# Optimization experiments

Hardware: AMD Instinct MI355X
Metric: run time of the kernel (lower is better)

Reference implementation:

```python
import jax, jax.numpy as jnp
import numpy as np

MARGIN = 0.2
BIG = 1e9  # sentinel for masked (positive-pair) entries in the row-min


def setup_inputs() -> dict:
    key = jax.random.key(0)
    k1, k2, k3 = jax.random.split(key, 3)
    B, D, NUM_CLASSES = 4096, 512, 1000
    z_s = jax.random.normal(k1, (B, D), dtype=jnp.float32)
    z_i = jax.random.normal(k2, (B, D), dtype=jnp.float32)
    labels = jax.random.randint(k3, (B,), 0, NUM_CLASSES, dtype=jnp.int64)
    return {"z_s": z_s, "z_i": z_i, "labels": labels}


def reference(z_s, z_i, labels):
    # dists[a, b] = 1 - <z_s[a], z_i[b]>   -- [B, B]
    dists = 1.0 - jnp.einsum("ad,bd->ab", z_s, z_i)
    pos_mask = labels[:, None] == labels[None, :]  # [B, B] same-label pairs

    p = jnp.diagonal(dists)  # positive distance per anchor, [B]
    # hardest negative per anchor: min over entries with different label
    n = jnp.min(jnp.where(pos_mask, BIG, dists), axis=1)  # [B]
    has_neg = ~jnp.all(pos_mask, axis=1)  # anchors with at least one negative

    per_anchor = jax.nn.relu(p - n + MARGIN)  # [B]
    count = jnp.sum(has_neg)
    total = jnp.sum(jnp.where(has_neg, per_anchor, 0.0))
    # mean over anchors that had negatives; 0.0 if none (matches torch fallback)
    return jnp.where(count > 0, total / jnp.maximum(count, 1).astype(total.dtype), 0.0)
```

## Files before the change

kernel.cpp:

```cpp
#include <hip/hip_runtime.h>
#include <hip/hip_bf16.h>

typedef __attribute__((ext_vector_type(8))) short bf16x8;
typedef __attribute__((ext_vector_type(4))) float f32x4;

#define NB 4096
#define ND 512
#define MARGIN_F 0.2f

__device__ __forceinline__ unsigned int enc_f32(float f) {
    unsigned int b = __float_as_uint(f);
    return (b & 0x80000000u) ? ~b : (b | 0x80000000u);
}

__device__ __forceinline__ float dec_f32(unsigned int e) {
    unsigned int b = (e & 0x80000000u) ? (e & 0x7fffffffu) : ~e;
    return __uint_as_float(b);
}

__device__ __forceinline__ void gld_lds16(const void* g, void* l) {
    __builtin_amdgcn_global_load_lds((__attribute__((address_space(1))) void*)g,
                                     (__attribute__((address_space(3))) void*)l,
                                     16, 0, 0);
}

__global__ __launch_bounds__(256) void k_prep(const float* __restrict__ zs,
                                              const float* __restrict__ zi,
                                              __hip_bfloat16* __restrict__ outb,
                                              unsigned int* __restrict__ rowmax) {
    const int bid = blockIdx.x;
    if (bid < 16) rowmax[bid * 256 + threadIdx.x] = 0u;

    int gid = bid * 256 + threadIdx.x;
    int mat = gid >> 18;
    int t   = gid & 0x3FFFF;
    int si  = t >> 6;
    int L   = t & 63;
    const float* src = mat ? zi : zs;
    int row = ((si >> 4) << 4) | (L & 15);
    int col = ((si & 15) << 5) | (((L >> 4) & 3) << 3);
    const float4* p = (const float4*)(src + (size_t)row * ND + col);
    float4 f0 = p[0];
    float4 f1 = p[1];
    union { __hip_bfloat16 h[8]; bf16x8 v; } u;
    u.h[0] = __float2bfloat16(f0.x);
    u.h[1] = __float2bfloat16(f0.y);
    u.h[2] = __float2bfloat16(f0.z);
    u.h[3] = __float2bfloat16(f0.w);
    u.h[4] = __float2bfloat16(f1.x);
    u.h[5] = __float2bfloat16(f1.y);
    u.h[6] = __float2bfloat16(f1.z);
    u.h[7] = __float2bfloat16(f1.w);
    bf16x8* dst = (bf16x8*)(outb + ((size_t)mat << 21) + ((size_t)si << 9) + (L << 3));
    *dst = u.v;
}

__global__ __launch_bounds__(256) void k_gemm_rowmax(const __hip_bfloat16* __restrict__ zsb,
                                                     const __hip_bfloat16* __restrict__ zib,
                                                     const int* __restrict__ labels,
                                                     unsigned int* __restrict__ rowmax,
                                                     float* __restrict__ p_diag) {
    __shared__ __align__(16) unsigned char sA[16384];
    __shared__ __align__(16) unsigned char sB[16384];
    __shared__ int labA[128];
    __shared__ int labB[128];

    const int tid = threadIdx.x;
    const int bx = blockIdx.x, by = blockIdx.y;

    if (tid < 128) labA[tid] = labels[by * 128 + tid];
    else           labB[tid - 128] = labels[bx * 128 + (tid - 128)];

    const char* gA = (const char*)zsb;
    const char* gB = (const char*)zib;
    const int rb0 = tid >> 7;
    const int rem = (tid & 127) << 4;
    size_t aStat[4], bStat[4];
#pragma unroll
    for (int rd = 0; rd < 4; ++rd) {
        int rb = rd * 2 + rb0;
        aStat[rd] = ((size_t)(by * 8 + rb) << 14) + rem;
        bStat[rd] = ((size_t)(bx * 8 + rb) << 14) + rem;
    }

    const int w = tid >> 6, lane = tid & 63;
    const int w_m = w >> 1, w_n = w & 1;
    const int fragOff = lane << 4;

    f32x4 acc[4][4];
#pragma unroll
    for (int i = 0; i < 4; ++i)
#pragma unroll
        for (int j = 0; j < 4; ++j)
            acc[i][j] = (f32x4){0.f, 0.f, 0.f, 0.f};

    for (int ks = 0; ks < 8; ++ks) {
        __syncthreads();
#pragma unroll
        for (int rd = 0; rd < 4; ++rd) {
            gld_lds16(gA + aStat[rd] + (size_t)ks * 2048, sA + rd * 4096 + (tid << 4));
            gld_lds16(gB + bStat[rd] + (size_t)ks * 2048, sB + rd * 4096 + (tid << 4));
        }
        __syncthreads();
#pragma unroll
        for (int kb = 0; kb < 2; ++kb) {
            bf16x8 af[4], bfr[4];
#pragma unroll
            for (int ms = 0; ms < 4; ++ms)
                af[ms] = *(const bf16x8*)(sA + (((w_m * 4 + ms) * 2 + kb) << 10) + fragOff);
#pragma unroll
            for (int ns = 0; ns < 4; ++ns)
                bfr[ns] = *(const bf16x8*)(sB + (((w_n * 4 + ns) * 2 + kb) << 10) + fragOff);
#pragma unroll
            for (int ms = 0; ms < 4; ++ms)
#pragma unroll
                for (int ns = 0; ns < 4; ++ns)
                    acc[ms][ns] = __builtin_amdgcn_mfma_f32_16x16x32_bf16(
                        af[ms], bfr[ns], acc[ms][ns], 0, 0, 0);
        }
    }

    const int quad = lane >> 4;
    const int lcol = lane & 15;

    int lb[4];
#pragma unroll
    for (int ns = 0; ns < 4; ++ns)
        lb[ns] = labB[w_n * 64 + ns * 16 + lcol];

#pragma unroll
    for (int ms = 0; ms < 4; ++ms) {
        int la[4];
#pragma unroll
        for (int r = 0; r < 4; ++r)
            la[r] = labA[w_m * 64 + ms * 16 + quad * 4 + r];
        float mx[4] = {-3.0e38f, -3.0e38f, -3.0e38f, -3.0e38f};
#pragma unroll
        for (int ns = 0; ns < 4; ++ns) {
#pragma unroll
            for (int r = 0; r < 4; ++r) {
                float v = acc[ms][ns][r];
                if (la[r] != lb[ns] && v > mx[r]) mx[r] = v;
            }
        }
#pragma unroll
        for (int r = 0; r < 4; ++r) {
            float m = mx[r];
            m = fmaxf(m, __shfl_xor(m, 1));
            m = fmaxf(m, __shfl_xor(m, 2));
            m = fmaxf(m, __shfl_xor(m, 4));
            m = fmaxf(m, __shfl_xor(m, 8));
            if (lcol == 0 && m > -2.9e38f) {
                int rowg = by * 128 + w_m * 64 + ms * 16 + quad * 4 + r;
                atomicMax(&rowmax[rowg], enc_f32(m));
            }
        }
    }

    if (bx == by && w_m == w_n) {
        int r = lcol - quad * 4;
        if (r >= 0 && r < 4) {
#pragma unroll
            for (int ms = 0; ms < 4; ++ms) {
                int rowg = by * 128 + w_m * 64 + ms * 16 + lcol;
                p_diag[rowg] = 1.0f - acc[ms][ms][r];
            }
        }
    }
}

__global__ __launch_bounds__(1024) void k_finalize(const unsigned int* __restrict__ rowmax,
                                                   const float* __restrict__ p_diag,
                                                   float* __restrict__ out) {
    int tid = threadIdx.x;
    float sum = 0.0f;
    int cnt = 0;
#pragma unroll
    for (int it = 0; it < 4; ++it) {
        int a = tid + it * 1024;
        unsigned int e = rowmax[a];
        if (e != 0u) {
            float n = 1.0f - dec_f32(e);
            float per = p_diag[a] - n + MARGIN_F;
            if (per > 0.0f) sum += per;
            cnt++;
        }
    }
#pragma unroll
    for (int off = 32; off > 0; off >>= 1) {
        sum += __shfl_xor(sum, off);
        cnt += __shfl_xor(cnt, off);
    }
    __shared__ float sSum[16];
    __shared__ int sCnt[16];
    int w = tid >> 6, lane = tid & 63;
    if (lane == 0) { sSum[w] = sum; sCnt[w] = cnt; }
    __syncthreads();
    if (tid == 0) {
        float ts = 0.0f;
        int tc = 0;
#pragma unroll
        for (int i = 0; i < 16; ++i) { ts += sSum[i]; tc += sCnt[i]; }
        out[0] = (tc > 0) ? ts / (float)tc : 0.0f;
    }
}

extern "C" void kernel_launch(void* const* d_in, const int* in_sizes, int n_in,
                              void* d_out, int out_size, void* d_ws, size_t ws_size,
                              hipStream_t stream) {
    (void)in_sizes; (void)n_in; (void)out_size; (void)ws_size;
    const float* zs = (const float*)d_in[0];
    const float* zi = (const float*)d_in[1];
    const int* labels = (const int*)d_in[2];
    float* out = (float*)d_out;

    char* ws = (char*)d_ws;
    __hip_bfloat16* zb = (__hip_bfloat16*)ws;
    unsigned int* rowmax = (unsigned int*)(ws + (8u << 20));
    float* p_diag = (float*)(ws + (8u << 20) + 16384);

    k_prep<<<2048, 256, 0, stream>>>(zs, zi, zb, rowmax);
    dim3 g(32, 32);
    k_gemm_rowmax<<<g, 256, 0, stream>>>(zb, zb + (size_t)NB * ND, labels, rowmax, p_diag);
    k_finalize<<<1, 1024, 0, stream>>>(rowmax, p_diag, out);
}
```

Before: 104.1 us.

## Use 256x256 tiles with double-buffered LDS pipeline and XCD-aware block mapping

```diff
diff --git a/kernel.cpp b/kernel.cpp
--- a/kernel.cpp
+++ b/kernel.cpp
@@ -23,6 +23,8 @@
                                      (__attribute__((address_space(3))) void*)l,
                                      16, 0, 0);
 }
+
+#define SBAR() asm volatile("s_barrier" ::: "memory")
 
 __global__ __launch_bounds__(256) void k_prep(const float* __restrict__ zs,
                                               const float* __restrict__ zi,
@@ -55,70 +57,126 @@
     *dst = u.v;
 }
 
-__global__ __launch_bounds__(256) void k_gemm_rowmax(const __hip_bfloat16* __restrict__ zsb,
-                                                     const __hip_bfloat16* __restrict__ zib,
-                                                     const int* __restrict__ labels,
-                                                     unsigned int* __restrict__ rowmax,
-                                                     float* __restrict__ p_diag) {
-    __shared__ __align__(16) unsigned char sA[16384];
-    __shared__ __align__(16) unsigned char sB[16384];
-    __shared__ int labA[128];
-    __shared__ int labB[128];
+__global__ __launch_bounds__(512, 2) void k_gemm_rowmax(const __hip_bfloat16* __restrict__ zsb,
+                                                        const __hip_bfloat16* __restrict__ zib,
+                                                        const int* __restrict__ labels,
+                                                        unsigned int* __restrict__ rowmax,
+                                                        float* __restrict__ p_diag) {
+    __shared__ __align__(16) unsigned char lds[131072];
+    __shared__ int labA[256];
+    __shared__ int labB[256];
 
     const int tid = threadIdx.x;
-    const int bx = blockIdx.x, by = blockIdx.y;
-
-    if (tid < 128) labA[tid] = labels[by * 128 + tid];
-    else           labB[tid - 128] = labels[bx * 128 + (tid - 128)];
+    const int bid = blockIdx.x;
+    const int xcd = bid & 7, lid = bid >> 3;
+    const int bx = ((xcd & 3) << 2) | (lid & 3);
+    const int by = ((xcd >> 2) << 3) | (lid >> 2);
+
+    if (tid < 256) labA[tid] = labels[by * 256 + tid];
+    else           labB[tid & 255] = labels[bx * 256 + (tid & 255)];
 
     const char* gA = (const char*)zsb;
     const char* gB = (const char*)zib;
-    const int rb0 = tid >> 7;
-    const int rem = (tid & 127) << 4;
-    size_t aStat[4], bStat[4];
-#pragma unroll
-    for (int rd = 0; rd < 4; ++rd) {
-        int rb = rd * 2 + rb0;
-        aStat[rd] = ((size_t)(by * 8 + rb) << 14) + rem;
-        bStat[rd] = ((size_t)(bx * 8 + rb) << 14) + rem;
-    }
+    const int inner = (tid & 127) << 4;
+    const int aB16 = by * 16 + (tid >> 7);
+    const int bB16 = bx * 16 + (tid >> 7);
+
+#define STAGE(kt, h) do {                                                          \
+        const char* _g = ((h) & 2) ? gB : gA;                                      \
+        int _rb = (((h) & 2) ? bB16 : aB16) + (((h) & 1) << 3);                    \
+        unsigned _ld = (((kt) & 1) << 16) + ((h) << 14) + (tid << 4);              \
+        gld_lds16(_g + (((size_t)_rb) << 14) + ((kt) << 11) + inner, lds + _ld);   \
+        gld_lds16(_g + (((size_t)(_rb + 4)) << 14) + ((kt) << 11) + inner,         \
+                  lds + _ld + 8192);                                               \
+    } while (0)
 
     const int w = tid >> 6, lane = tid & 63;
-    const int w_m = w >> 1, w_n = w & 1;
-    const int fragOff = lane << 4;
-
-    f32x4 acc[4][4];
-#pragma unroll
-    for (int i = 0; i < 4; ++i)
+    const int w_m = w >> 2, w_n = w & 3;
+    const unsigned fragOff = (unsigned)(lane << 4);
+    const unsigned aBase = (unsigned)(w_m << 14) + fragOff;
+    const unsigned bBase = 32768u + (unsigned)((w_n >> 1) << 14)
+                         + (unsigned)(((w_n & 1) << 2) << 11) + fragOff;
+
+    f32x4 acc[8][4];
+#pragma unroll
+    for (int i = 0; i < 8; ++i)
 #pragma unroll
         for (int j = 0; j < 4; ++j)
             acc[i][j] = (f32x4){0.f, 0.f, 0.f, 0.f};
 
-    for (int ks = 0; ks < 8; ++ks) {
-        __syncthreads();
-#pragma unroll
-        for (int rd = 0; rd < 4; ++rd) {
-            gld_lds16(gA + aStat[rd] + (size_t)ks * 2048, sA + rd * 4096 + (tid << 4));
-            gld_lds16(gB + bStat[rd] + (size_t)ks * 2048, sB + rd * 4096 + (tid << 4));
-        }
-        __syncthreads();
-#pragma unroll
-        for (int kb = 0; kb < 2; ++kb) {
-            bf16x8 af[4], bfr[4];
-#pragma unroll
-            for (int ms = 0; ms < 4; ++ms)
-                af[ms] = *(const bf16x8*)(sA + (((w_m * 4 + ms) * 2 + kb) << 10) + fragOff);
-#pragma unroll
-            for (int ns = 0; ns < 4; ++ns)
-                bfr[ns] = *(const bf16x8*)(sB + (((w_n * 4 + ns) * 2 + kb) << 10) + fragOff);
-#pragma unroll
-            for (int ms = 0; ms < 4; ++ms)
-#pragma unroll
-                for (int ns = 0; ns < 4; ++ns)
-                    acc[ms][ns] = __builtin_amdgcn_mfma_f32_16x16x32_bf16(
-                        af[ms], bfr[ns], acc[ms][ns], 0, 0, 0);
-        }
-    }
+    STAGE(0, 0); STAGE(0, 1); STAGE(0, 2); STAGE(0, 3);
+    STAGE(1, 0); STAGE(1, 1);
+    __syncthreads();
+
+#pragma unroll
+    for (int kt = 0; kt < 8; ++kt) {
+        const unsigned par = (unsigned)((kt & 1) << 16);
+        bf16x8 a0[8], a1[8], b0[4], b1[4];
+
+#pragma unroll
+        for (int ms = 0; ms < 8; ++ms)
+            a0[ms] = *(const bf16x8*)(lds + par + aBase + (ms << 11));
+#pragma unroll
+        for (int ns = 0; ns < 4; ++ns)
+            b0[ns] = *(const bf16x8*)(lds + par + bBase + (ns << 11));
+        if (kt < 7) STAGE(kt + 1, 2);
+        __builtin_amdgcn_s_setprio(1);
+#pragma unroll
+        for (int ms = 0; ms < 8; ++ms)
+            acc[ms][0] = __builtin_amdgcn_mfma_f32_16x16x32_bf16(a0[ms], b0[0], acc[ms][0], 0, 0, 0);
+#pragma unroll
+        for (int ms = 0; ms < 8; ++ms)
+            acc[ms][1] = __builtin_amdgcn_mfma_f32_16x16x32_bf16(a0[ms], b0[1], acc[ms][1], 0, 0, 0);
+        __builtin_amdgcn_s_setprio(0);
+        SBAR();
+
+#pragma unroll
+        for (int ms = 0; ms < 8; ++ms)
+            a1[ms] = *(const bf16x8*)(lds + par + aBase + (ms << 11) + 1024);
+        if (kt < 7) STAGE(kt + 1, 3);
+        __builtin_amdgcn_s_setprio(1);
+#pragma unroll
+        for (int ms = 0; ms < 8; ++ms)
+            acc[ms][2] = __builtin_amdgcn_mfma_f32_16x16x32_bf16(a0[ms], b0[2], acc[ms][2], 0, 0, 0);
+#pragma unroll
+        for (int ms = 0; ms < 8; ++ms)
+            acc[ms][3] = __builtin_amdgcn_mfma_f32_16x16x32_bf16(a0[ms], b0[3], acc[ms][3], 0, 0, 0);
+        __builtin_amdgcn_s_setprio(0);
+        asm volatile("s_waitcnt lgkmcnt(0)" ::: "memory");
+        SBAR();
+
+#pragma unroll
+        for (int ns = 0; ns < 4; ++ns)
+            b1[ns] = *(const bf16x8*)(lds + par + bBase + (ns << 11) + 1024);
+        if (kt < 6) STAGE(kt + 2, 0);
+        __builtin_amdgcn_s_setprio(1);
+#pragma unroll
+        for (int ms = 0; ms < 8; ++ms)
+            acc[ms][0] = __builtin_amdgcn_mfma_f32_16x16x32_bf16(a1[ms], b1[0], acc[ms][0], 0, 0, 0);
+#pragma unroll
+        for (int ms = 0; ms < 8; ++ms)
+            acc[ms][1] = __builtin_amdgcn_mfma_f32_16x16x32_bf16(a1[ms], b1[1], acc[ms][1], 0, 0, 0);
+        __builtin_amdgcn_s_setprio(0);
+        SBAR();
+
+        if (kt < 6) STAGE(kt + 2, 1);
+        __builtin_amdgcn_s_setprio(1);
+#pragma unroll
+        for (int ms = 0; ms < 8; ++ms)
+            acc[ms][2] = __builtin_amdgcn_mfma_f32_16x16x32_bf16(a1[ms], b1[2], acc[ms][2], 0, 0, 0);
+#pragma unroll
+        for (int ms = 0; ms < 8; ++ms)
+            acc[ms][3] = __builtin_amdgcn_mfma_f32_16x16x32_bf16(a1[ms], b1[3], acc[ms][3], 0, 0, 0);
+        __builtin_amdgcn_s_setprio(0);
+        if (kt < 6) {
+            asm volatile("s_waitcnt vmcnt(4)" ::: "memory");
+            SBAR();
+        } else if (kt == 6) {
+            asm volatile("s_waitcnt vmcnt(0)" ::: "memory");
+            SBAR();
+        }
+    }
+#undef STAGE
 
     const int quad = lane >> 4;
     const int lcol = lane & 15;
@@ -129,11 +187,11 @@
         lb[ns] = labB[w_n * 64 + ns * 16 + lcol];
 
 #pragma unroll
-    for (int ms = 0; ms < 4; ++ms) {
+    for (int ms = 0; ms < 8; ++ms) {
         int la[4];
 #pragma unroll
         for (int r = 0; r < 4; ++r)
-            la[r] = labA[w_m * 64 + ms * 16 + quad * 4 + r];
+            la[r] = labA[w_m * 128 + ms * 16 + quad * 4 + r];
         float mx[4] = {-3.0e38f, -3.0e38f, -3.0e38f, -3.0e38f};
 #pragma unroll
         for (int ns = 0; ns < 4; ++ns) {
@@ -151,19 +209,20 @@
             m = fmaxf(m, __shfl_xor(m, 4));
             m = fmaxf(m, __shfl_xor(m, 8));
             if (lcol == 0 && m > -2.9e38f) {
-                int rowg = by * 128 + w_m * 64 + ms * 16 + quad * 4 + r;
+                int rowg = by * 256 + w_m * 128 + ms * 16 + quad * 4 + r;
                 atomicMax(&rowmax[rowg], enc_f32(m));
             }
         }
     }
 
-    if (bx == by && w_m == w_n) {
+    if (bx == by && (w_n >> 1) == w_m) {
         int r = lcol - quad * 4;
         if (r >= 0 && r < 4) {
 #pragma unroll
-            for (int ms = 0; ms < 4; ++ms) {
-                int rowg = by * 128 + w_m * 64 + ms * 16 + lcol;
-                p_diag[rowg] = 1.0f - acc[ms][ms][r];
+            for (int ns = 0; ns < 4; ++ns) {
+                int ms = ((w_n & 1) << 2) + ns;
+                int rowg = by * 256 + w_m * 128 + ms * 16 + lcol;
+                p_diag[rowg] = 1.0f - acc[ms][ns][r];
             }
         }
     }
@@ -220,7 +279,6 @@
     float* p_diag = (float*)(ws + (8u << 20) + 16384);
 
     k_prep<<<2048, 256, 0, stream>>>(zs, zi, zb, rowmax);
-    dim3 g(32, 32);
-    k_gemm_rowmax<<<g, 256, 0, stream>>>(zb, zb + (size_t)NB * ND, labels, rowmax, p_diag);
+    k_gemm_rowmax<<<256, 512, 0, stream>>>(zb, zb + (size_t)NB * ND, labels, rowmax, p_diag);
     k_finalize<<<1, 1024, 0, stream>>>(rowmax, p_diag, out);
 }
```

Measured after the change: 237.3 us. 128% more time.
